# Kernel optimization log

Measured on AMD Instinct MI355X. Metric: run time of the kernel, lower is better.

The kernel has to match this reference:

```python
import jax, jax.numpy as jnp
import numpy as np

V, S, E, H, D, L = 32000, 1024, 512, 8, 64, 4
FF = 4 * E
EPS = 1e-5


def setup_inputs() -> dict:
    key = jax.random.key(0)
    ks = jax.random.split(key, 24)
    s = 0.02
    inp = {
        "x": jax.random.randint(ks[0], (2, S), 0, V, dtype=jnp.int32),
        "tok_emb": jax.random.normal(ks[1], (V, E), jnp.float32) * s,
        "pos_emb": jax.random.normal(ks[2], (S, E), jnp.float32) * s,
        "Wq": jax.random.normal(ks[3], (L, H, E, D), jnp.float32) * s,
        "bq": jnp.zeros((L, H, D), jnp.float32),
        "Wk": jax.random.normal(ks[4], (L, H, E, D), jnp.float32) * s,
        "bk": jnp.zeros((L, H, D), jnp.float32),
        "Wv": jax.random.normal(ks[5], (L, H, E, D), jnp.float32) * s,
        "bv": jnp.zeros((L, H, D), jnp.float32),
        "Wo": jax.random.normal(ks[6], (L, H * D, E), jnp.float32) * s,
        "bo": jnp.zeros((L, E), jnp.float32),
        "W1": jax.random.normal(ks[7], (L, E, FF), jnp.float32) * s,
        "b1": jnp.zeros((L, FF), jnp.float32),
        "W2": jax.random.normal(ks[8], (L, FF, E), jnp.float32) * s,
        "b2": jnp.zeros((L, E), jnp.float32),
        "ln1_g": jnp.ones((L, E), jnp.float32),
        "ln1_b": jnp.zeros((L, E), jnp.float32),
        "ln2_g": jnp.ones((L, E), jnp.float32),
        "ln2_b": jnp.zeros((L, E), jnp.float32),
        "Wout": jax.random.normal(ks[9], (E, V), jnp.float32) * s,
        "bout": jnp.zeros((V,), jnp.float32),
    }
    return inp


def _layernorm(x, g, b):
    mu = jnp.mean(x, axis=-1, keepdims=True)
    var = jnp.mean(jnp.square(x - mu), axis=-1, keepdims=True)
    return (x - mu) * jax.lax.rsqrt(var + EPS) * g + b


def _decoder(h, Wq, bq, Wk, bk, Wv, bv, Wo, bo, W1, b1, W2, b2, g1, be1, g2, be2):
    B, T, _ = h.shape
    # per-head Q/K/V projections, batched over heads (matches concat of per-head linears)
    Q = jnp.einsum("bse,hed->bhsd", h, Wq) + bq[None, :, None, :]
    K = jnp.einsum("bse,hed->bhsd", h, Wk) + bk[None, :, None, :]
    Vv = jnp.einsum("bse,hed->bhsd", h, Wv) + bv[None, :, None, :]
    scores = jnp.einsum("bhqd,bhkd->bhqk", Q, K) / jnp.sqrt(jnp.asarray(D, h.dtype))
    causal = jnp.tril(jnp.ones((T, T), bool))
    scores = jnp.where(causal[None, None], scores, -jnp.inf)
    attn = jax.nn.softmax(scores, axis=-1)
    out = jnp.einsum("bhqk,bhkd->bhqd", attn, Vv)
    conc = out.transpose(0, 2, 1, 3).reshape(B, T, H * D)  # concat heads along feature dim
    mha = conc @ Wo + bo
    ln = _layernorm(h + mha, g1, be1)
    ff = jax.nn.relu(ln @ W1 + b1) @ W2 + b2
    return _layernorm(ln + ff, g2, be2)


def reference(x, tok_emb, pos_emb, Wq, bq, Wk, bk, Wv, bv, Wo, bo,
              W1, b1, W2, b2, ln1_g, ln1_b, ln2_g, ln2_b, Wout, bout):
    B, T = x.shape
    h = tok_emb[x] + pos_emb[:T][None]  # [B,T,E]
    for l in range(L):
        h = _decoder(h, Wq[l], bq[l], Wk[l], bk[l], Wv[l], bv[l], Wo[l], bo[l],
                     W1[l], b1[l], W2[l], b2[l], ln1_g[l], ln1_b[l], ln2_g[l], ln2_b[l])
    return h @ Wout + bout  # [B,T,V] logits
```

## Files before the change

### kernel.cpp

```cpp
#include <hip/hip_runtime.h>
#include <hip/hip_bf16.h>


#define B_ 2
#define S_ 1024
#define E_ 512
#define H_ 8
#define D_ 64
#define L_ 4
#define FF_ 2048
#define V_ 32000
#define M_ (B_ * S_)
#define QKV_N (3 * H_ * D_)

typedef __attribute__((ext_vector_type(8))) short short8;
typedef __attribute__((ext_vector_type(8))) ushort ushort8;
typedef __attribute__((ext_vector_type(4))) float f32x4;

__device__ __forceinline__ float b2f(ushort u) {
  union { uint32_t i; float f; } c; c.i = ((uint32_t)u) << 16; return c.f;
}
__device__ __forceinline__ ushort f2b(float f) {
  union { float f; uint32_t i; } c; c.f = f;
  uint32_t u = c.i;
  return (ushort)((u + 0x7FFFu + ((u >> 16) & 1u)) >> 16);
}

__device__ __forceinline__ void gload16(const ushort* g, ushort* l) {
  __builtin_amdgcn_global_load_lds(
      (const __attribute__((address_space(1))) void*)g,
      (__attribute__((address_space(3))) void*)l, 16, 0, 0);
}

__global__ __launch_bounds__(256) void setup_kernel(
    const int* __restrict__ x, const float* __restrict__ tok,
    const float* __restrict__ pos, float* __restrict__ hf, ushort* __restrict__ hb,
    const float* __restrict__ Wq, const float* __restrict__ Wk,
    const float* __restrict__ Wv, ushort* __restrict__ wqkv,
    const float* __restrict__ Wo, ushort* __restrict__ wo_t,
    const float* __restrict__ W1, ushort* __restrict__ w1_t,
    const float* __restrict__ W2, ushort* __restrict__ w2_t,
    const float* __restrict__ Wout, ushort* __restrict__ wout_t,
    const float* __restrict__ bq, const float* __restrict__ bk,
    const float* __restrict__ bv, float* __restrict__ bqkv) {
  __shared__ float tile[32][33];
  int bz = blockIdx.x;
  int tid = threadIdx.x;

  auto tr32 = [&](const float* in, ushort* out, int inC, int R, int r0, int c0) {
    int tx = tid & 31, ty = tid >> 5;
#pragma unroll
    for (int i = 0; i < 4; i++)
      tile[ty + 8 * i][tx] = in[(size_t)(r0 + ty + 8 * i) * inC + c0 + tx];
    __syncthreads();
#pragma unroll
    for (int i = 0; i < 4; i++)
      out[(size_t)(c0 + ty + 8 * i) * R + r0 + tx] = f2b(tile[tx][ty + 8 * i]);
  };

  if (bz < 4096) {
    int idx = bz * 256 + tid;
    int e = idx & (E_ - 1);
    int t = (idx >> 9) & (S_ - 1);
    int b = idx >> 19;
    int tokid = x[b * S_ + t];
    float v = tok[(size_t)tokid * E_ + e] + pos[(size_t)t * E_ + e];
    hf[idx] = v;
    hb[idx] = f2b(v);
  } else if (bz < 7168) {
    int li = bz - 4096;
    int batch = li >> 5, q = li & 31;
    int t = batch / (L_ * H_);
    int rem = batch % (L_ * H_);
    int lyr = rem / H_, h = rem % H_;
    const float* in = ((t == 0) ? Wq : (t == 1) ? Wk : Wv) +
                      ((size_t)lyr * H_ + h) * E_ * D_;
    ushort* out = wqkv + (size_t)lyr * QKV_N * E_ + ((size_t)t * 512 + h * 64) * E_;
    tr32(in, out, D_, E_, (q & 15) * 32, (q >> 4) * 32);
  } else if (bz < 8192) {
    int li = bz - 7168;
    int lyr = li >> 8, q = li & 255;
    tr32(Wo + (size_t)lyr * E_ * E_, wo_t + (size_t)lyr * E_ * E_, E_, E_,
         (q & 15) * 32, (q >> 4) * 32);
  } else if (bz < 12288) {
    int li = bz - 8192;
    int lyr = li >> 10, q = li & 1023;
    tr32(W1 + (size_t)lyr * E_ * FF_, w1_t + (size_t)lyr * FF_ * E_, FF_, E_,
         (q & 15) * 32, (q >> 4) * 32);
  } else if (bz < 16384) {
    int li = bz - 12288;
    int lyr = li >> 10, q = li & 1023;
    tr32(W2 + (size_t)lyr * FF_ * E_, w2_t + (size_t)lyr * E_ * FF_, E_, FF_,
         (q & 63) * 32, (q >> 6) * 32);
  } else if (bz < 32384) {
    int li = bz - 16384;
    tr32(Wout, wout_t, V_, E_, (li & 15) * 32, (li >> 4) * 32);
  } else {
    int idx = (bz - 32384) * 256 + tid;
    if (idx < L_ * QKV_N) {
      int n = idx % QKV_N;
      int lyr = idx / QKV_N;
      int t = n / (H_ * D_);
      int hd = n % (H_ * D_);
      const float* src = (t == 0) ? bq : (t == 1) ? bk : bv;
      bqkv[idx] = src[(size_t)lyr * H_ * D_ + hd];
    }
  }
}

template <bool OUTBF, bool RELU, bool VT>
__global__ __launch_bounds__(256) void mfma_gemm_kernel(
    const ushort* __restrict__ A, const ushort* __restrict__ Bt,
    const float* __restrict__ bias, const float* __restrict__ resid,
    void* __restrict__ out, ushort* __restrict__ vt,
    int M, int N, int K, int gx) {
  __shared__ __align__(16) ushort As[3 * 8192];
  __shared__ __align__(16) ushort Bs[3 * 8192];
  int tid = threadIdx.x;
  int w = tid >> 6, l = tid & 63;
  int wr = w >> 1, wc = w & 1;
  int lane15 = l & 15, lhi = l >> 4;

  int bid = blockIdx.x;
  int bx = bid % gx, by = bid / gx;
  int row0 = by * 128, col0 = bx * 128;

  int rr8 = l >> 3;
  int ksrc = (((l & 7) ^ rr8) << 3);
  const ushort *gA[2][2], *gB[2][2];
  int lofs[2][2];
#pragma unroll
  for (int cc = 0; cc < 2; cc++) {
    int c = w + cc * 4;
#pragma unroll
    for (int h = 0; h < 2; h++) {
      int row = c * 16 + h * 8 + rr8;
      gA[cc][h] = A + (size_t)(row0 + row) * K + ksrc;
      gB[cc][h] = Bt + (size_t)(col0 + row) * K + ksrc;
      lofs[cc][h] = c * 1024 + h * 512 + l * 8;
    }
  }

  f32x4 acc[4][4] = {};
  int nt = K >> 6;

  auto stage = [&](int buf, int t) {
    int k0 = t << 6;
    int ob = buf * 8192;
#pragma unroll
    for (int cc = 0; cc < 2; cc++)
#pragma unroll
      for (int h = 0; h < 2; h++) {
        gload16(gA[cc][h] + k0, &As[ob + lofs[cc][h]]);
        gload16(gB[cc][h] + k0, &Bs[ob + lofs[cc][h]]);
      }
  };
  auto compute = [&](int buf) {
    int ob = buf * 8192;
    int sa = (lane15 & 7) << 4;
    short8 a[4][2], b[4][2];
#pragma unroll
    for (int i = 0; i < 4; i++) {
      int ra = ob + (wr * 64 + i * 16 + lane15) * 64;
      int rb = ob + (wc * 64 + i * 16 + lane15) * 64;
#pragma unroll
      for (int kk = 0; kk < 2; kk++) {
        int inner = ((kk * 64 + lhi * 16) ^ sa) >> 1;
        a[i][kk] = *(const short8*)&As[ra + inner];
        b[i][kk] = *(const short8*)&Bs[rb + inner];
      }
    }
#pragma unroll
    for (int i = 0; i < 4; i++)
#pragma unroll
      for (int j = 0; j < 4; j++) {
        acc[i][j] = __builtin_amdgcn_mfma_f32_16x16x32_bf16(a[i][0], b[j][0], acc[i][j], 0, 0, 0);
        acc[i][j] = __builtin_amdgcn_mfma_f32_16x16x32_bf16(a[i][1], b[j][1], acc[i][j], 0, 0, 0);
      }
  };

  stage(0, 0);
  stage(1, 1);
  for (int t = 0; t < nt; t++) {
    if (t + 2 < nt) {
      stage((t + 2) % 3, t + 2);
      __builtin_amdgcn_sched_barrier(0);
      asm volatile("s_waitcnt vmcnt(16)" ::: "memory");
    } else if (t + 1 < nt) {
      __builtin_amdgcn_sched_barrier(0);
      asm volatile("s_waitcnt vmcnt(8)" ::: "memory");
    } else {
      __builtin_amdgcn_sched_barrier(0);
      asm volatile("s_waitcnt vmcnt(0)" ::: "memory");
    }
    __builtin_amdgcn_s_barrier();
    __builtin_amdgcn_sched_barrier(0);
    __builtin_amdgcn_s_setprio(1);
    compute(t % 3);
    __builtin_amdgcn_s_setprio(0);
    __builtin_amdgcn_sched_barrier(0);
    __builtin_amdgcn_s_barrier();
  }

  float* outf = (float*)out;
  ushort* outb = (ushort*)out;
#pragma unroll
  for (int i = 0; i < 4; i++) {
    int gr = row0 + wr * 64 + i * 16 + lhi * 4;
#pragma unroll
    for (int j = 0; j < 4; j++) {
      int gc = col0 + wc * 64 + j * 16 + lane15;
      float bb = bias[gc];
#pragma unroll
      for (int r = 0; r < 4; r++) {
        float v = acc[i][j][r] + bb;
        if (resid) v += resid[(size_t)(gr + r) * N + gc];
        if (RELU) v = fmaxf(v, 0.f);
        if (VT && gc >= 1024) {
          int d = gc - 1024;
          int grr = gr + r;
          int bb2 = grr >> 10, s = grr & 1023;
          vt[(((size_t)(bb2 * 8 + (d >> 6)) * 64 + (d & 63)) << 10) + s] = f2b(v);
        } else if (OUTBF) {
          outb[(size_t)(gr + r) * N + gc] = f2b(v);
        } else {
          outf[(size_t)(gr + r) * N + gc] = v;
        }
      }
    }
  }
}

template <int SK>
__global__ __launch_bounds__(256) void mfma_gemm_sk_kernel(
    const ushort* __restrict__ A, const ushort* __restrict__ Bt,
    ushort* __restrict__ part, int M, int N, int K, int gx) {
  __shared__ __align__(16) ushort As[3 * 8192];
  __shared__ __align__(16) ushort Bs[3 * 8192];
  int tid = threadIdx.x;
  int w = tid >> 6, l = tid & 63;
  int wr = w >> 1, wc = w & 1;
  int lane15 = l & 15, lhi = l >> 4;

  int tiles = gx * (M >> 7);
  int sk = blockIdx.x / tiles;
  int rem = blockIdx.x % tiles;
  int bx = rem % gx, by = rem / gx;
  int row0 = by * 128, col0 = bx * 128;
  int klen = K / SK, kbeg = sk * klen;

  int rr8 = l >> 3;
  int ksrc = (((l & 7) ^ rr8) << 3);
  const ushort *gA[2][2], *gB[2][2];
  int lofs[2][2];
#pragma unroll
  for (int cc = 0; cc < 2; cc++) {
    int c = w + cc * 4;
#pragma unroll
    for (int h = 0; h < 2; h++) {
      int row = c * 16 + h * 8 + rr8;
      gA[cc][h] = A + (size_t)(row0 + row) * K + kbeg + ksrc;
      gB[cc][h] = Bt + (size_t)(col0 + row) * K + kbeg + ksrc;
      lofs[cc][h] = c * 1024 + h * 512 + l * 8;
    }
  }

  f32x4 acc[4][4] = {};
  int nt = klen >> 6;

  auto stage = [&](int buf, int t) {
    int k0 = t << 6;
    int ob = buf * 8192;
#pragma unroll
    for (int cc = 0; cc < 2; cc++)
#pragma unroll
      for (int h = 0; h < 2; h++) {
        gload16(gA[cc][h] + k0, &As[ob + lofs[cc][h]]);
        gload16(gB[cc][h] + k0, &Bs[ob + lofs[cc][h]]);
      }
  };
  auto compute = [&](int buf) {
    int ob = buf * 8192;
    int sa = (lane15 & 7) << 4;
    short8 a[4][2], b[4][2];
#pragma unroll
    for (int i = 0; i < 4; i++) {
      int ra = ob + (wr * 64 + i * 16 + lane15) * 64;
      int rb = ob + (wc * 64 + i * 16 + lane15) * 64;
#pragma unroll
      for (int kk = 0; kk < 2; kk++) {
        int inner = ((kk * 64 + lhi * 16) ^ sa) >> 1;
        a[i][kk] = *(const short8*)&As[ra + inner];
        b[i][kk] = *(const short8*)&Bs[rb + inner];
      }
    }
#pragma unroll
    for (int i = 0; i < 4; i++)
#pragma unroll
      for (int j = 0; j < 4; j++) {
        acc[i][j] = __builtin_amdgcn_mfma_f32_16x16x32_bf16(a[i][0], b[j][0], acc[i][j], 0, 0, 0);
        acc[i][j] = __builtin_amdgcn_mfma_f32_16x16x32_bf16(a[i][1], b[j][1], acc[i][j], 0, 0, 0);
      }
  };

  stage(0, 0);
  if (nt > 1) stage(1, 1);
  for (int t = 0; t < nt; t++) {
    if (t + 2 < nt) {
      stage((t + 2) % 3, t + 2);
      __builtin_amdgcn_sched_barrier(0);
      asm volatile("s_waitcnt vmcnt(16)" ::: "memory");
    } else if (t + 1 < nt) {
      __builtin_amdgcn_sched_barrier(0);
      asm volatile("s_waitcnt vmcnt(8)" ::: "memory");
    } else {
      __builtin_amdgcn_sched_barrier(0);
      asm volatile("s_waitcnt vmcnt(0)" ::: "memory");
    }
    __builtin_amdgcn_s_barrier();
    __builtin_amdgcn_sched_barrier(0);
    __builtin_amdgcn_s_setprio(1);
    compute(t % 3);
    __builtin_amdgcn_s_setprio(0);
    __builtin_amdgcn_sched_barrier(0);
    __builtin_amdgcn_s_barrier();
  }

  ushort* dst = part + (size_t)sk * M * N;
#pragma unroll
  for (int i = 0; i < 4; i++) {
    int gr = row0 + wr * 64 + i * 16 + lhi * 4;
#pragma unroll
    for (int j = 0; j < 4; j++) {
      int gc = col0 + wc * 64 + j * 16 + lane15;
#pragma unroll
      for (int r = 0; r < 4; r++)
        dst[(size_t)(gr + r) * N + gc] = f2b(acc[i][j][r]);
    }
  }
}

__global__ __launch_bounds__(512) void gemm_fin_kernel(
    const ushort* __restrict__ A, const ushort* __restrict__ Bt,
    const float* __restrict__ bias, float* __restrict__ out) {
  constexpr int K = E_, N = V_, NT = E_ / 64;
  __shared__ __align__(16) ushort As[2][128 * 64];
  __shared__ __align__(16) ushort Bs[3][256 * 64];
  int tid = threadIdx.x;
  int w = tid >> 6, l = tid & 63;
  int wr = w >> 2, wc = w & 3;
  int lane15 = l & 15, lhi = l >> 4;

  int bid = blockIdx.x;
  int wg = (bid & 7) * 250 + (bid >> 3);
  int by = wg & 15, bx = wg >> 4;
  int row0 = by * 128, col0 = bx * 256;

  const ushort* ga[2]; int la[2];
  const ushort* gb[4]; int lb[4];
#pragma unroll
  for (int p = 0; p < 2; p++) {
    int i = p * 512 + tid;
    int row = i >> 3, kg = i & 7;
    ga[p] = A + (size_t)(row0 + row) * K + ((kg ^ (row & 7)) << 3);
    la[p] = i * 8;
  }
#pragma unroll
  for (int p = 0; p < 4; p++) {
    int i = p * 512 + tid;
    int row = i >> 3, kg = i & 7;
    gb[p] = Bt + (size_t)(col0 + row) * K + ((kg ^ (row & 7)) << 3);
    lb[p] = i * 8;
  }

  f32x4 acc[4][4] = {};

  auto stageA = [&](int buf, int t) {
    int k0 = t << 6;
#pragma unroll
    for (int p = 0; p < 2; p++) gload16(ga[p] + k0, &As[buf][la[p]]);
  };
  auto stageB = [&](int buf, int t) {
    int k0 = t << 6;
#pragma unroll
    for (int p = 0; p < 4; p++) gload16(gb[p] + k0, &Bs[buf][lb[p]]);
  };
  auto compute = [&](int ba, int bb) {
    int sa = (lane15 & 7) << 4;
#pragma unroll
    for (int kk = 0; kk < 2; kk++) {
      int inner = ((kk * 64 + lhi * 16) ^ sa) >> 1;
      short8 a[4], b[4];
#pragma unroll
      for (int i = 0; i < 4; i++)
        a[i] = *(const short8*)&As[ba][(wr * 64 + i * 16 + lane15) * 64 + inner];
#pragma unroll
      for (int j = 0; j < 4; j++)
        b[j] = *(const short8*)&Bs[bb][(wc * 64 + j * 16 + lane15) * 64 + inner];
#pragma unroll
      for (int i = 0; i < 4; i++)
#pragma unroll
        for (int j = 0; j < 4; j++)
          acc[i][j] = __builtin_amdgcn_mfma_f32_16x16x32_bf16(a[i], b[j], acc[i][j], 0, 0, 0);
    }
  };

  stageA(0, 0);
  stageB(0, 0);
  stageB(1, 1);
  __builtin_amdgcn_sched_barrier(0);
  asm volatile("s_waitcnt vmcnt(4)" ::: "memory");
  __builtin_amdgcn_s_barrier();
  __builtin_amdgcn_sched_barrier(0);

#pragma unroll
  for (int t = 0; t < NT; t++) {
    if (t + 1 < NT) stageA((t + 1) & 1, t + 1);
    if (t + 2 < NT) stageB((t + 2) % 3, t + 2);
    __builtin_amdgcn_s_setprio(1);
    compute(t & 1, t % 3);
    __builtin_amdgcn_s_setprio(0);
    if (t + 1 < NT) {
      __builtin_amdgcn_sched_barrier(0);
      if (t + 2 < NT) asm volatile("s_waitcnt vmcnt(4)" ::: "memory");
      else            asm volatile("s_waitcnt vmcnt(0)" ::: "memory");
      __builtin_amdgcn_s_barrier();
      __builtin_amdgcn_sched_barrier(0);
    }
  }

#pragma unroll
  for (int i = 0; i < 4; i++) {
    int gr = row0 + wr * 64 + i * 16 + lhi * 4;
#pragma unroll
    for (int j = 0; j < 4; j++) {
      int gc = col0 + wc * 64 + j * 16 + lane15;
      float bb = bias[gc];
#pragma unroll
      for (int r = 0; r < 4; r++)
        __builtin_nontemporal_store(acc[i][j][r] + bb,
                                    &out[(size_t)(gr + r) * N + gc]);
    }
  }
}

__global__ __launch_bounds__(64) void fattn_kernel(
    const ushort* __restrict__ qkv, const ushort* __restrict__ vt,
    ushort* __restrict__ conc) {
  int qb = blockIdx.x;
  int bh = blockIdx.y;
  int b = bh >> 3, h = bh & 7;
  int l = threadIdx.x;
  int lane15 = l & 15, lhi = l >> 4;

  __shared__ __align__(16) ushort plds[16][72];

  const ushort* kbase = qkv + (size_t)b * S_ * QKV_N + 512 + h * 64;
  const ushort* vbase = vt + (size_t)bh * 64 * S_;

#pragma unroll
  for (int pass = 0; pass < 2; pass++) {
    int tile = pass ? (63 - qb) : qb;
    int q0 = tile * 16;
    int qtop = q0 + 15;

    const ushort* qr = qkv + (size_t)(b * S_ + q0 + lane15) * QKV_N + h * 64;
    short8 qf0 = *(const short8*)(qr + lhi * 8);
    short8 qf1 = *(const short8*)(qr + 32 + lhi * 8);

    f32x4 o[4] = {};
    float lsum[4] = {0.f, 0.f, 0.f, 0.f};

    for (int kv0 = 0; kv0 <= qtop; kv0 += 64) {
      float pr[4][4];
#pragma unroll
      for (int t = 0; t < 4; t++) {
        if (kv0 + t * 16 <= qtop) {
          const ushort* kr = kbase + (size_t)(kv0 + t * 16 + lane15) * QKV_N;
          short8 kf0 = *(const short8*)(kr + lhi * 8);
          short8 kf1 = *(const short8*)(kr + 32 + lhi * 8);
          f32x4 s = {};
          s = __builtin_amdgcn_mfma_f32_16x16x32_bf16(qf0, kf0, s, 0, 0, 0);
          s = __builtin_amdgcn_mfma_f32_16x16x32_bf16(qf1, kf1, s, 0, 0, 0);
          int kidx = kv0 + t * 16 + lane15;
#pragma unroll
          for (int r = 0; r < 4; r++) {
            float p = (kidx > q0 + lhi * 4 + r) ? 0.f : __expf(s[r] * 0.125f);
            pr[t][r] = p;
            plds[lhi * 4 + r][t * 16 + lane15] = f2b(p);
          }
        } else {
#pragma unroll
          for (int r = 0; r < 4; r++) {
            pr[t][r] = 0.f;
            plds[lhi * 4 + r][t * 16 + lane15] = 0;
          }
        }
      }
#pragma unroll
      for (int r = 0; r < 4; r++) {
        float rs = (pr[0][r] + pr[1][r]) + (pr[2][r] + pr[3][r]);
        rs += __shfl_xor(rs, 1);
        rs += __shfl_xor(rs, 2);
        rs += __shfl_xor(rs, 4);
        rs += __shfl_xor(rs, 8);
        lsum[r] += rs;
      }
      short8 pa0 = *(const short8*)&plds[lane15][lhi * 8];
      short8 pa1 = *(const short8*)&plds[lane15][32 + lhi * 8];
#pragma unroll
      for (int n = 0; n < 4; n++) {
        const ushort* vr = vbase + (size_t)(n * 16 + lane15) * S_ + kv0;
        short8 vf0 = *(const short8*)(vr + lhi * 8);
        short8 vf1 = *(const short8*)(vr + 32 + lhi * 8);
        o[n] = __builtin_amdgcn_mfma_f32_16x16x32_bf16(pa0, vf0, o[n], 0, 0, 0);
        o[n] = __builtin_amdgcn_mfma_f32_16x16x32_bf16(pa1, vf1, o[n], 0, 0, 0);
      }
    }
#pragma unroll
    for (int r = 0; r < 4; r++) {
      float inv = 1.f / lsum[r];
      int row = b * S_ + q0 + lhi * 4 + r;
#pragma unroll
      for (int n = 0; n < 4; n++)
        conc[(size_t)row * (H_ * D_) + h * 64 + n * 16 + lane15] = f2b(o[n][r] * inv);
    }
  }
}

template <int SK>
__global__ __launch_bounds__(256) void ln_red_kernel(
    const ushort* __restrict__ part, const float* __restrict__ bias,
    const float* __restrict__ resid, const float* __restrict__ g,
    const float* __restrict__ bsh, float* __restrict__ outf,
    ushort* __restrict__ outb) {
  int w = threadIdx.x >> 6, l = threadIdx.x & 63;
  int row = blockIdx.x * 4 + w;
  size_t off = (size_t)row * E_ + l * 8;
  float4 r0 = *(const float4*)(resid + off);
  float4 r1 = *(const float4*)(resid + off + 4);
  float4 bb0 = *(const float4*)(bias + l * 8);
  float4 bb1 = *(const float4*)(bias + l * 8 + 4);
  float x[8] = {r0.x + bb0.x, r0.y + bb0.y, r0.z + bb0.z, r0.w + bb0.w,
                r1.x + bb1.x, r1.y + bb1.y, r1.z + bb1.z, r1.w + bb1.w};
#pragma unroll
  for (int s = 0; s < SK; s++) {
    ushort8 pv = *(const ushort8*)(part + (size_t)s * M_ * E_ + off);
#pragma unroll
    for (int i = 0; i < 8; i++) x[i] += b2f(pv[i]);
  }
  float s = 0.f, q = 0.f;
#pragma unroll
  for (int i = 0; i < 8; i++) { s += x[i]; q += x[i] * x[i]; }
#pragma unroll
  for (int off2 = 1; off2 < 64; off2 <<= 1) {
    s += __shfl_xor(s, off2);
    q += __shfl_xor(q, off2);
  }
  float mu = s * (1.f / 512.f);
  float var = q * (1.f / 512.f) - mu * mu;
  float rs = rsqrtf(var + 1e-5f);
  float4 g0 = *(const float4*)(g + l * 8);
  float4 g1 = *(const float4*)(g + l * 8 + 4);
  float4 b0 = *(const float4*)(bsh + l * 8);
  float4 b1 = *(const float4*)(bsh + l * 8 + 4);
  float gg[8] = {g0.x, g0.y, g0.z, g0.w, g1.x, g1.y, g1.z, g1.w};
  float bbv[8] = {b0.x, b0.y, b0.z, b0.w, b1.x, b1.y, b1.z, b1.w};
  float y[8];
#pragma unroll
  for (int i = 0; i < 8; i++) y[i] = (x[i] - mu) * rs * gg[i] + bbv[i];
  float* of = outf + off;
  *(float4*)of = make_float4(y[0], y[1], y[2], y[3]);
  *(float4*)(of + 4) = make_float4(y[4], y[5], y[6], y[7]);
  ushort4 u0 = {f2b(y[0]), f2b(y[1]), f2b(y[2]), f2b(y[3])};
  ushort4 u1 = {f2b(y[4]), f2b(y[5]), f2b(y[6]), f2b(y[7])};
  ushort* ob = outb + off;
  *(ushort4*)ob = u0;
  *(ushort4*)(ob + 4) = u1;
}

extern "C" void kernel_launch(void* const* d_in, const int* in_sizes, int n_in,
                              void* d_out, int out_size, void* d_ws, size_t ws_size,
                              hipStream_t stream) {
  const int* x = (const int*)d_in[0];
  const float* tok = (const float*)d_in[1];
  const float* pos = (const float*)d_in[2];
  const float* Wq = (const float*)d_in[3];
  const float* bq = (const float*)d_in[4];
  const float* Wk = (const float*)d_in[5];
  const float* bk = (const float*)d_in[6];
  const float* Wv = (const float*)d_in[7];
  const float* bv = (const float*)d_in[8];
  const float* Wo = (const float*)d_in[9];
  const float* bo = (const float*)d_in[10];
  const float* W1 = (const float*)d_in[11];
  const float* b1 = (const float*)d_in[12];
  const float* W2 = (const float*)d_in[13];
  const float* b2 = (const float*)d_in[14];
  const float* ln1g = (const float*)d_in[15];
  const float* ln1b = (const float*)d_in[16];
  const float* ln2g = (const float*)d_in[17];
  const float* ln2b = (const float*)d_in[18];
  const float* Wout = (const float*)d_in[19];
  const float* bout = (const float*)d_in[20];
  float* out = (float*)d_out;

  char* p = (char*)d_ws;
  auto alloc = [&](size_t bytes) {
    char* r = p;
    p += (bytes + 255) & ~(size_t)255;
    return r;
  };
  float* h_f = (float*)alloc((size_t)M_ * E_ * 4);
  ushort* h_b = (ushort*)alloc((size_t)M_ * E_ * 2);
  ushort* qkv_b = (ushort*)alloc((size_t)M_ * QKV_N * 2);
  ushort* conc_b = (ushort*)alloc((size_t)M_ * E_ * 2);
  ushort* part = (ushort*)alloc((size_t)4 * M_ * E_ * 2);
  float* ln_f = (float*)alloc((size_t)M_ * E_ * 4);
  ushort* ln_b = (ushort*)alloc((size_t)M_ * E_ * 2);
  ushort* ff_b = (ushort*)alloc((size_t)M_ * FF_ * 2);
  ushort* vt_b = (ushort*)alloc((size_t)B_ * H_ * D_ * S_ * 2);
  ushort* wqkv = (ushort*)alloc((size_t)L_ * QKV_N * E_ * 2);
  float* bqkv = (float*)alloc((size_t)L_ * QKV_N * 4);
  ushort* wo_t = (ushort*)alloc((size_t)L_ * E_ * E_ * 2);
  ushort* w1_t = (ushort*)alloc((size_t)L_ * FF_ * E_ * 2);
  ushort* w2_t = (ushort*)alloc((size_t)L_ * E_ * FF_ * 2);
  ushort* wout_t = (ushort*)alloc((size_t)V_ * E_ * 2);

  setup_kernel<<<32408, 256, 0, stream>>>(
      x, tok, pos, h_f, h_b, Wq, Wk, Wv, wqkv, Wo, wo_t, W1, w1_t,
      W2, w2_t, Wout, wout_t, bq, bk, bv, bqkv);

  for (int l = 0; l < L_; ++l) {
    mfma_gemm_kernel<true, false, true><<<(QKV_N / 128) * (M_ / 128), 256, 0, stream>>>(
        h_b, wqkv + (size_t)l * QKV_N * E_, bqkv + l * QKV_N, nullptr,
        qkv_b, vt_b, M_, QKV_N, E_, QKV_N / 128);
    fattn_kernel<<<dim3(S_ / 32, B_ * H_), 64, 0, stream>>>(qkv_b, vt_b, conc_b);
    mfma_gemm_sk_kernel<4><<<4 * (E_ / 128) * (M_ / 128), 256, 0, stream>>>(
        conc_b, wo_t + (size_t)l * E_ * E_, part, M_, E_, E_, E_ / 128);
    ln_red_kernel<4><<<M_ / 4, 256, 0, stream>>>(
        part, bo + l * E_, h_f, ln1g + l * E_, ln1b + l * E_, ln_f, ln_b);
    mfma_gemm_kernel<true, true, false><<<(FF_ / 128) * (M_ / 128), 256, 0, stream>>>(
        ln_b, w1_t + (size_t)l * FF_ * E_, b1 + l * FF_, nullptr, ff_b, nullptr,
        M_, FF_, E_, FF_ / 128);
    mfma_gemm_sk_kernel<4><<<4 * (E_ / 128) * (M_ / 128), 256, 0, stream>>>(
        ff_b, w2_t + (size_t)l * E_ * FF_, part, M_, E_, FF_, E_ / 128);
    ln_red_kernel<4><<<M_ / 4, 256, 0, stream>>>(
        part, b2 + l * E_, ln_f, ln2g + l * E_, ln2b + l * E_, h_f, h_b);
  }

  gemm_fin_kernel<<<(M_ / 128) * (V_ / 256), 512, 0, stream>>>(
      h_b, wout_t, bout, out);
}
```

Baseline: 542.7 us.

## Single-barrier GEMM pipeline and cheaper causal softmax row sums in attention

In both GEMM mainloops, the next tile's prefetch now issues right after the per-iteration barrier instead of before the wait. The trailing barrier is removed, so each k-step synchronizes once using the three-buffer ring. The wait counts are simplified to match. In attention, key tiles lying entirely below the diagonal skip the per-element causal compare, and the per-row exp sums stay per lane, with the cross-lane shuffle reduction done once after the KV loop instead of every block. This cuts barriers and shuffle work, but depends on the buffer-reuse ordering staying correct with one barrier per step.

```diff
diff --git a/kernel.cpp b/kernel.cpp
--- a/kernel.cpp
+++ b/kernel.cpp
@@ -182,24 +182,15 @@
   stage(0, 0);
   stage(1, 1);
   for (int t = 0; t < nt; t++) {
-    if (t + 2 < nt) {
-      stage((t + 2) % 3, t + 2);
-      __builtin_amdgcn_sched_barrier(0);
-      asm volatile("s_waitcnt vmcnt(16)" ::: "memory");
-    } else if (t + 1 < nt) {
-      __builtin_amdgcn_sched_barrier(0);
-      asm volatile("s_waitcnt vmcnt(8)" ::: "memory");
-    } else {
-      __builtin_amdgcn_sched_barrier(0);
-      asm volatile("s_waitcnt vmcnt(0)" ::: "memory");
-    }
+    __builtin_amdgcn_sched_barrier(0);
+    if (t + 1 < nt) asm volatile("s_waitcnt vmcnt(8)" ::: "memory");
+    else            asm volatile("s_waitcnt vmcnt(0)" ::: "memory");
     __builtin_amdgcn_s_barrier();
     __builtin_amdgcn_sched_barrier(0);
+    if (t + 2 < nt) stage((t + 2) % 3, t + 2);
     __builtin_amdgcn_s_setprio(1);
     compute(t % 3);
     __builtin_amdgcn_s_setprio(0);
-    __builtin_amdgcn_sched_barrier(0);
-    __builtin_amdgcn_s_barrier();
   }
 
   float* outf = (float*)out;
@@ -306,24 +297,15 @@
   stage(0, 0);
   if (nt > 1) stage(1, 1);
   for (int t = 0; t < nt; t++) {
-    if (t + 2 < nt) {
-      stage((t + 2) % 3, t + 2);
-      __builtin_amdgcn_sched_barrier(0);
-      asm volatile("s_waitcnt vmcnt(16)" ::: "memory");
-    } else if (t + 1 < nt) {
-      __builtin_amdgcn_sched_barrier(0);
-      asm volatile("s_waitcnt vmcnt(8)" ::: "memory");
-    } else {
-      __builtin_amdgcn_sched_barrier(0);
-      asm volatile("s_waitcnt vmcnt(0)" ::: "memory");
-    }
+    __builtin_amdgcn_sched_barrier(0);
+    if (t + 1 < nt) asm volatile("s_waitcnt vmcnt(8)" ::: "memory");
+    else            asm volatile("s_waitcnt vmcnt(0)" ::: "memory");
     __builtin_amdgcn_s_barrier();
     __builtin_amdgcn_sched_barrier(0);
+    if (t + 2 < nt) stage((t + 2) % 3, t + 2);
     __builtin_amdgcn_s_setprio(1);
     compute(t % 3);
     __builtin_amdgcn_s_setprio(0);
-    __builtin_amdgcn_sched_barrier(0);
-    __builtin_amdgcn_s_barrier();
   }
 
   ushort* dst = part + (size_t)sk * M * N;
@@ -472,39 +454,37 @@
     float lsum[4] = {0.f, 0.f, 0.f, 0.f};
 
     for (int kv0 = 0; kv0 <= qtop; kv0 += 64) {
-      float pr[4][4];
 #pragma unroll
       for (int t = 0; t < 4; t++) {
-        if (kv0 + t * 16 <= qtop) {
-          const ushort* kr = kbase + (size_t)(kv0 + t * 16 + lane15) * QKV_N;
+        int kb = kv0 + t * 16;
+        if (kb <= qtop) {
+          const ushort* kr = kbase + (size_t)(kb + lane15) * QKV_N;
           short8 kf0 = *(const short8*)(kr + lhi * 8);
           short8 kf1 = *(const short8*)(kr + 32 + lhi * 8);
           f32x4 s = {};
           s = __builtin_amdgcn_mfma_f32_16x16x32_bf16(qf0, kf0, s, 0, 0, 0);
           s = __builtin_amdgcn_mfma_f32_16x16x32_bf16(qf1, kf1, s, 0, 0, 0);
-          int kidx = kv0 + t * 16 + lane15;
-#pragma unroll
-          for (int r = 0; r < 4; r++) {
-            float p = (kidx > q0 + lhi * 4 + r) ? 0.f : __expf(s[r] * 0.125f);
-            pr[t][r] = p;
-            plds[lhi * 4 + r][t * 16 + lane15] = f2b(p);
+          if (kb + 15 <= q0) {
+#pragma unroll
+            for (int r = 0; r < 4; r++) {
+              float p = __expf(s[r] * 0.125f);
+              lsum[r] += p;
+              plds[lhi * 4 + r][t * 16 + lane15] = f2b(p);
+            }
+          } else {
+            int kidx = kb + lane15;
+#pragma unroll
+            for (int r = 0; r < 4; r++) {
+              float p = (kidx > q0 + lhi * 4 + r) ? 0.f : __expf(s[r] * 0.125f);
+              lsum[r] += p;
+              plds[lhi * 4 + r][t * 16 + lane15] = f2b(p);
+            }
           }
         } else {
 #pragma unroll
-          for (int r = 0; r < 4; r++) {
-            pr[t][r] = 0.f;
+          for (int r = 0; r < 4; r++)
             plds[lhi * 4 + r][t * 16 + lane15] = 0;
-          }
         }
-      }
-#pragma unroll
-      for (int r = 0; r < 4; r++) {
-        float rs = (pr[0][r] + pr[1][r]) + (pr[2][r] + pr[3][r]);
-        rs += __shfl_xor(rs, 1);
-        rs += __shfl_xor(rs, 2);
-        rs += __shfl_xor(rs, 4);
-        rs += __shfl_xor(rs, 8);
-        lsum[r] += rs;
       }
       short8 pa0 = *(const short8*)&plds[lane15][lhi * 8];
       short8 pa1 = *(const short8*)&plds[lane15][32 + lhi * 8];
@@ -516,6 +496,13 @@
         o[n] = __builtin_amdgcn_mfma_f32_16x16x32_bf16(pa0, vf0, o[n], 0, 0, 0);
         o[n] = __builtin_amdgcn_mfma_f32_16x16x32_bf16(pa1, vf1, o[n], 0, 0, 0);
       }
+    }
+#pragma unroll
+    for (int r = 0; r < 4; r++) {
+      lsum[r] += __shfl_xor(lsum[r], 1);
+      lsum[r] += __shfl_xor(lsum[r], 2);
+      lsum[r] += __shfl_xor(lsum[r], 4);
+      lsum[r] += __shfl_xor(lsum[r], 8);
     }
 #pragma unroll
     for (int r = 0; r < 4; r++) {
```

Measured after the change: 558.8 us. 3.0% more time.

## Fuse split-K reduction and LayerNorm into split-K GEMM via last-block counter

Applied to the files above, without the earlier changes.

The separate ln_red kernels are removed. Each split-K GEMM block now increments a per-row-band atomic counter after writing its partial tile. The last of the 16 blocks for a 128-row band sums the partials, adds bias and residual, and applies LayerNorm for those rows. This removes 8 kernel launches and their launch gaps, at the cost of a serialized tail. The LayerNorm work for each row band runs in a single block, using 4 waves over 128 rows.

```diff
diff --git a/kernel.cpp b/kernel.cpp
--- a/kernel.cpp
+++ b/kernel.cpp
@@ -42,7 +42,8 @@
     const float* __restrict__ W2, ushort* __restrict__ w2_t,
     const float* __restrict__ Wout, ushort* __restrict__ wout_t,
     const float* __restrict__ bq, const float* __restrict__ bk,
-    const float* __restrict__ bv, float* __restrict__ bqkv) {
+    const float* __restrict__ bv, float* __restrict__ bqkv,
+    int* __restrict__ ctr) {
   __shared__ float tile[32][33];
   int bz = blockIdx.x;
   int tid = threadIdx.x;
@@ -95,8 +96,11 @@
   } else if (bz < 32384) {
     int li = bz - 16384;
     tr32(Wout, wout_t, V_, E_, (li & 15) * 32, (li >> 4) * 32);
+  } else if (bz == 32384) {
+    int idx = tid;
+    if (idx < 16) ctr[idx] = 0;
   } else {
-    int idx = (bz - 32384) * 256 + tid;
+    int idx = (bz - 32385) * 256 + tid;
     if (idx < L_ * QKV_N) {
       int n = idx % QKV_N;
       int lyr = idx / QKV_N;
@@ -232,11 +236,16 @@
 }
 
 template <int SK>
-__global__ __launch_bounds__(256) void mfma_gemm_sk_kernel(
+__global__ __launch_bounds__(256) void mfma_gemm_sk_ln_kernel(
     const ushort* __restrict__ A, const ushort* __restrict__ Bt,
-    ushort* __restrict__ part, int M, int N, int K, int gx) {
+    ushort* __restrict__ part, int* __restrict__ ctr,
+    const float* __restrict__ bias, const float* __restrict__ resid,
+    const float* __restrict__ g, const float* __restrict__ bsh,
+    float* __restrict__ outf, ushort* __restrict__ outb,
+    int M, int N, int K, int gx) {
   __shared__ __align__(16) ushort As[3 * 8192];
   __shared__ __align__(16) ushort Bs[3 * 8192];
+  __shared__ int s_last;
   int tid = threadIdx.x;
   int w = tid >> 6, l = tid & 63;
   int wr = w >> 1, wc = w & 1;
@@ -337,6 +346,63 @@
       for (int r = 0; r < 4; r++)
         dst[(size_t)(gr + r) * N + gc] = f2b(acc[i][j][r]);
     }
+  }
+
+  asm volatile("s_waitcnt vmcnt(0)" ::: "memory");
+  __syncthreads();
+  if (tid == 0) {
+    __threadfence();
+    int old = atomicAdd(&ctr[by], 1);
+    s_last = (old == SK * 4 - 1);
+    if (s_last) ctr[by] = 0;
+  }
+  __syncthreads();
+  if (!s_last) return;
+  __threadfence();
+
+  for (int rr = w; rr < 128; rr += 4) {
+    int row = row0 + rr;
+    size_t off = (size_t)row * N + l * 8;
+    float4 r0 = *(const float4*)(resid + off);
+    float4 r1 = *(const float4*)(resid + off + 4);
+    float4 bb0 = *(const float4*)(bias + l * 8);
+    float4 bb1 = *(const float4*)(bias + l * 8 + 4);
+    float x[8] = {r0.x + bb0.x, r0.y + bb0.y, r0.z + bb0.z, r0.w + bb0.w,
+                  r1.x + bb1.x, r1.y + bb1.y, r1.z + bb1.z, r1.w + bb1.w};
+#pragma unroll
+    for (int s = 0; s < SK; s++) {
+      ushort8 pv = *(const ushort8*)(part + (size_t)s * M * N + off);
+#pragma unroll
+      for (int i = 0; i < 8; i++) x[i] += b2f(pv[i]);
+    }
+    float sm = 0.f, q = 0.f;
+#pragma unroll
+    for (int i = 0; i < 8; i++) { sm += x[i]; q += x[i] * x[i]; }
+#pragma unroll
+    for (int off2 = 1; off2 < 64; off2 <<= 1) {
+      sm += __shfl_xor(sm, off2);
+      q += __shfl_xor(q, off2);
+    }
+    float mu = sm * (1.f / 512.f);
+    float var = q * (1.f / 512.f) - mu * mu;
+    float rs = rsqrtf(var + 1e-5f);
+    float4 g0 = *(const float4*)(g + l * 8);
+    float4 g1 = *(const float4*)(g + l * 8 + 4);
+    float4 b0 = *(const float4*)(bsh + l * 8);
+    float4 b1 = *(const float4*)(bsh + l * 8 + 4);
+    float gg[8] = {g0.x, g0.y, g0.z, g0.w, g1.x, g1.y, g1.z, g1.w};
+    float bbv[8] = {b0.x, b0.y, b0.z, b0.w, b1.x, b1.y, b1.z, b1.w};
+    float y[8];
+#pragma unroll
+    for (int i = 0; i < 8; i++) y[i] = (x[i] - mu) * rs * gg[i] + bbv[i];
+    float* of = outf + off;
+    *(float4*)of = make_float4(y[0], y[1], y[2], y[3]);
+    *(float4*)(of + 4) = make_float4(y[4], y[5], y[6], y[7]);
+    ushort4 u0 = {f2b(y[0]), f2b(y[1]), f2b(y[2]), f2b(y[3])};
+    ushort4 u1 = {f2b(y[4]), f2b(y[5]), f2b(y[6]), f2b(y[7])};
+    ushort* ob = outb + off;
+    *(ushort4*)ob = u0;
+    *(ushort4*)(ob + 4) = u1;
   }
 }
 
@@ -526,57 +592,6 @@
         conc[(size_t)row * (H_ * D_) + h * 64 + n * 16 + lane15] = f2b(o[n][r] * inv);
     }
   }
-}
-
-template <int SK>
-__global__ __launch_bounds__(256) void ln_red_kernel(
-    const ushort* __restrict__ part, const float* __restrict__ bias,
-    const float* __restrict__ resid, const float* __restrict__ g,
-    const float* __restrict__ bsh, float* __restrict__ outf,
-    ushort* __restrict__ outb) {
-  int w = threadIdx.x >> 6, l = threadIdx.x & 63;
-  int row = blockIdx.x * 4 + w;
-  size_t off = (size_t)row * E_ + l * 8;
-  float4 r0 = *(const float4*)(resid + off);
-  float4 r1 = *(const float4*)(resid + off + 4);
-  float4 bb0 = *(const float4*)(bias + l * 8);
-  float4 bb1 = *(const float4*)(bias + l * 8 + 4);
-  float x[8] = {r0.x + bb0.x, r0.y + bb0.y, r0.z + bb0.z, r0.w + bb0.w,
-                r1.x + bb1.x, r1.y + bb1.y, r1.z + bb1.z, r1.w + bb1.w};
-#pragma unroll
-  for (int s = 0; s < SK; s++) {
-    ushort8 pv = *(const ushort8*)(part + (size_t)s * M_ * E_ + off);
-#pragma unroll
-    for (int i = 0; i < 8; i++) x[i] += b2f(pv[i]);
-  }
-  float s = 0.f, q = 0.f;
-#pragma unroll
-  for (int i = 0; i < 8; i++) { s += x[i]; q += x[i] * x[i]; }
-#pragma unroll
-  for (int off2 = 1; off2 < 64; off2 <<= 1) {
-    s += __shfl_xor(s, off2);
-    q += __shfl_xor(q, off2);
-  }
-  float mu = s * (1.f / 512.f);
-  float var = q * (1.f / 512.f) - mu * mu;
-  float rs = rsqrtf(var + 1e-5f);
-  float4 g0 = *(const float4*)(g + l * 8);
-  float4 g1 = *(const float4*)(g + l * 8 + 4);
-  float4 b0 = *(const float4*)(bsh + l * 8);
-  float4 b1 = *(const float4*)(bsh + l * 8 + 4);
-  float gg[8] = {g0.x, g0.y, g0.z, g0.w, g1.x, g1.y, g1.z, g1.w};
-  float bbv[8] = {b0.x, b0.y, b0.z, b0.w, b1.x, b1.y, b1.z, b1.w};
-  float y[8];
-#pragma unroll
-  for (int i = 0; i < 8; i++) y[i] = (x[i] - mu) * rs * gg[i] + bbv[i];
-  float* of = outf + off;
-  *(float4*)of = make_float4(y[0], y[1], y[2], y[3]);
-  *(float4*)(of + 4) = make_float4(y[4], y[5], y[6], y[7]);
-  ushort4 u0 = {f2b(y[0]), f2b(y[1]), f2b(y[2]), f2b(y[3])};
-  ushort4 u1 = {f2b(y[4]), f2b(y[5]), f2b(y[6]), f2b(y[7])};
-  ushort* ob = outb + off;
-  *(ushort4*)ob = u0;
-  *(ushort4*)(ob + 4) = u1;
 }
 
 extern "C" void kernel_launch(void* const* d_in, const int* in_sizes, int n_in,
@@ -616,6 +631,7 @@
   ushort* qkv_b = (ushort*)alloc((size_t)M_ * QKV_N * 2);
   ushort* conc_b = (ushort*)alloc((size_t)M_ * E_ * 2);
   ushort* part = (ushort*)alloc((size_t)4 * M_ * E_ * 2);
+  int* ctr = (int*)alloc(64);
   float* ln_f = (float*)alloc((size_t)M_ * E_ * 4);
   ushort* ln_b = (ushort*)alloc((size_t)M_ * E_ * 2);
   ushort* ff_b = (ushort*)alloc((size_t)M_ * FF_ * 2);
@@ -627,26 +643,24 @@
   ushort* w2_t = (ushort*)alloc((size_t)L_ * E_ * FF_ * 2);
   ushort* wout_t = (ushort*)alloc((size_t)V_ * E_ * 2);
 
-  setup_kernel<<<32408, 256, 0, stream>>>(
+  setup_kernel<<<32409, 256, 0, stream>>>(
       x, tok, pos, h_f, h_b, Wq, Wk, Wv, wqkv, Wo, wo_t, W1, w1_t,
-      W2, w2_t, Wout, wout_t, bq, bk, bv, bqkv);
+      W2, w2_t, Wout, wout_t, bq, bk, bv, bqkv, ctr);
 
   for (int l = 0; l < L_; ++l) {
     mfma_gemm_kernel<true, false, true><<<(QKV_N / 128) * (M_ / 128), 256, 0, stream>>>(
         h_b, wqkv + (size_t)l * QKV_N * E_, bqkv + l * QKV_N, nullptr,
         qkv_b, vt_b, M_, QKV_N, E_, QKV_N / 128);
     fattn_kernel<<<dim3(S_ / 32, B_ * H_), 64, 0, stream>>>(qkv_b, vt_b, conc_b);
-    mfma_gemm_sk_kernel<4><<<4 * (E_ / 128) * (M_ / 128), 256, 0, stream>>>(
-        conc_b, wo_t + (size_t)l * E_ * E_, part, M_, E_, E_, E_ / 128);
-    ln_red_kernel<4><<<M_ / 4, 256, 0, stream>>>(
-        part, bo + l * E_, h_f, ln1g + l * E_, ln1b + l * E_, ln_f, ln_b);
+    mfma_gemm_sk_ln_kernel<4><<<4 * (E_ / 128) * (M_ / 128), 256, 0, stream>>>(
+        conc_b, wo_t + (size_t)l * E_ * E_, part, ctr, bo + l * E_, h_f,
+        ln1g + l * E_, ln1b + l * E_, ln_f, ln_b, M_, E_, E_, E_ / 128);
     mfma_gemm_kernel<true, true, false><<<(FF_ / 128) * (M_ / 128), 256, 0, stream>>>(
         ln_b, w1_t + (size_t)l * FF_ * E_, b1 + l * FF_, nullptr, ff_b, nullptr,
         M_, FF_, E_, FF_ / 128);
-    mfma_gemm_sk_kernel<4><<<4 * (E_ / 128) * (M_ / 128), 256, 0, stream>>>(
-        ff_b, w2_t + (size_t)l * E_ * FF_, part, M_, E_, FF_, E_ / 128);
-    ln_red_kernel<4><<<M_ / 4, 256, 0, stream>>>(
-        part, b2 + l * E_, ln_f, ln2g + l * E_, ln2b + l * E_, h_f, h_b);
+    mfma_gemm_sk_ln_kernel<4><<<4 * (E_ / 128) * (M_ / 128), 256, 0, stream>>>(
+        ff_b, w2_t + (size_t)l * E_ * FF_, part, ctr, b2 + l * E_, ln_f,
+        ln2g + l * E_, ln2b + l * E_, h_f, h_b, M_, E_, FF_, E_ / 128);
   }
 
   gemm_fin_kernel<<<(M_ / 128) * (V_ / 256), 512, 0, stream>>>(
```

Result: slower. 800.7 us (+47.5%).
